# Optimization experiments

Measured on AMD Instinct MI355X. Metric: run time of the kernel, lower is better.

The kernel has to match this reference:

```python
import jax, jax.numpy as jnp
import numpy as np


def setup_inputs() -> dict:
    key = jax.random.key(0)
    k1, k2, k3, k4 = jax.random.split(key, 4)
    B1, N1, B2, N2, D = 64, 128, 64, 128, 128
    v1 = jax.random.normal(k1, (B1, N1, D), dtype=jnp.float32)
    v2 = jax.random.normal(k2, (B2, N2, D), dtype=jnp.float32)
    sz1 = jax.random.randint(k3, (B1,), 0, 128, dtype=jnp.int64)
    sz2 = jax.random.randint(k4, (B2,), 0, 128, dtype=jnp.int64)
    return {"v1": v1, "sz1": sz1, "v2": v2, "sz2": sz2}


def reference(v1, sz1, v2, sz2):
    # v1: (B1, N1, D) padded node features; v2: (B2, N2, D)
    # Pairwise Euclidean distances dist[b1,b2,i,j] = ||v1[b1,i] - v2[b2,j]||
    # via the gemm identity instead of the original's 5D broadcast.
    x2 = jnp.sum(v1 * v1, axis=-1)                     # (B1, N1)
    y2 = jnp.sum(v2 * v2, axis=-1)                     # (B2, N2)
    xy = jnp.einsum('aid,bjd->abij', v1, v2)           # (B1, B2, N1, N2)
    sq = x2[:, None, :, None] + y2[None, :, None, :] - 2.0 * xy
    dist = jnp.sqrt(jnp.maximum(sq, 0.0))              # (B1, B2, N1, N2)

    N1, N2 = v1.shape[1], v2.shape[1]
    mask1 = jnp.arange(N1)[None, :] >= sz1[:, None]    # (B1, N1) padded v1 nodes
    mask2 = jnp.arange(N2)[None, :] >= sz2[:, None]    # (B2, N2) padded v2 nodes
    mask = mask1[:, None, :, None] | mask2[None, :, None, :]  # (B1, B2, N1, N2)

    # Original fills masked entries with the global max of the (unmasked) distances.
    maximum = dist.max()
    dm = jnp.where(mask, maximum, dist)

    bm1 = dm.min(axis=2)                               # min over v1 nodes -> (B1, B2, N2)
    bm2 = dm.min(axis=3)                               # min over v2 nodes -> (B1, B2, N1)
    bm1 = jnp.where(jnp.all(mask, axis=2), 0.0, bm1)   # zero fully-masked columns
    bm2 = jnp.where(jnp.all(mask, axis=3), 0.0, bm2)   # zero fully-masked rows

    return bm1.sum(axis=2) + bm2.sum(axis=2)           # (B1, B2)
```

## Files before the change

kernel.cpp:

```cpp
#include <hip/hip_runtime.h>
#include <math.h>


typedef __attribute__((ext_vector_type(8))) short short8;
typedef __attribute__((ext_vector_type(4))) float f32x4;
typedef unsigned int u32;
typedef unsigned short ushort_t;

static __device__ __forceinline__ ushort_t f32_to_bf16_rne(float f) {
    u32 b = __float_as_uint(f);
    b += 0x7FFFu + ((b >> 16) & 1u);
    return (ushort_t)(b >> 16);
}

__global__ __launch_bounds__(256) void softhd_pre(
    const float* __restrict__ v1, const float* __restrict__ v2,
    ushort_t* __restrict__ v1b, ushort_t* __restrict__ v2b,
    float* __restrict__ x2g, float* __restrict__ y2g)
{
    int flat = blockIdx.x * 256 + threadIdx.x;
    int c = flat & 15;
    int r = (flat >> 4) & 127;
    int b = (flat >> 11) & 63;
    int t = flat >> 17;

    const float* src = (t ? v2 : v1) + ((size_t)((b << 7) + r) << 7) + c * 8;
    char* dstp = (char*)((t ? v2b : v1b) + ((size_t)b << 14));

    float4 q0 = *(const float4*)(src);
    float4 q1 = *(const float4*)(src + 4);

    ushort_t h[8];
    h[0] = f32_to_bf16_rne(q0.x); h[1] = f32_to_bf16_rne(q0.y);
    h[2] = f32_to_bf16_rne(q0.z); h[3] = f32_to_bf16_rne(q0.w);
    h[4] = f32_to_bf16_rne(q1.x); h[5] = f32_to_bf16_rne(q1.y);
    h[6] = f32_to_bf16_rne(q1.z); h[7] = f32_to_bf16_rne(q1.w);

    float p = 0.f;
#pragma unroll
    for (int k = 0; k < 8; ++k) {
        float fv = __uint_as_float((u32)h[k] << 16);
        p += fv * fv;
    }

    uint4 w;
    w.x = (u32)h[0] | ((u32)h[1] << 16);
    w.y = (u32)h[2] | ((u32)h[3] << 16);
    w.z = (u32)h[4] | ((u32)h[5] << 16);
    w.w = (u32)h[6] | ((u32)h[7] << 16);

    int off = ((c >> 2) << 13) + ((r >> 3) << 9) + ((c & 3) << 7) + ((r & 7) << 4);
    *(uint4*)(dstp + off) = w;

    p += __shfl_xor(p, 1);
    p += __shfl_xor(p, 2);
    p += __shfl_xor(p, 4);
    p += __shfl_xor(p, 8);
    if (c == 0) (t ? y2g : x2g)[(b << 7) + r] = p;
}

__global__ __launch_bounds__(256, 4) void softhd_mfma(
    const ushort_t* __restrict__ v1b, const ushort_t* __restrict__ v2b,
    const float* __restrict__ x2g, const float* __restrict__ y2g,
    const int* __restrict__ sz1, const int* __restrict__ sz2,
    float* __restrict__ out)
{
    __shared__ __align__(16) ushort_t sb[2][2][4096];
    __shared__ float sx2[128], sy2[128];
    __shared__ u32 sbm1[128], sbm2[128];
    __shared__ float swsum[4];

    const int tid = threadIdx.x;
    const int lane = tid & 63;
    const int wid = tid >> 6;
    const int bid = ((blockIdx.x & 7) << 9) | (blockIdx.x >> 3);
    const int b1 = bid >> 6, b2 = bid & 63;

    const char* gp0 = (const char*)(v1b + ((size_t)b1 << 14));
    const char* gp1 = (const char*)(v2b + ((size_t)b2 << 14));

#define STAGE(d, q)                                                          \
    {                                                                        \
        _Pragma("unroll")                                                    \
        for (int e = 0; e < 2; ++e) {                                        \
            int m16 = ((e << 8) + tid) << 4;                                 \
            __builtin_amdgcn_global_load_lds(                                \
                (const __attribute__((address_space(1))) u32*)(gp0 + ((q) << 13) + m16), \
                (__attribute__((address_space(3))) u32*)((char*)&sb[d][0][0] + m16),     \
                16, 0, 0);                                                   \
            __builtin_amdgcn_global_load_lds(                                \
                (const __attribute__((address_space(1))) u32*)(gp1 + ((q) << 13) + m16), \
                (__attribute__((address_space(3))) u32*)((char*)&sb[d][1][0] + m16),     \
                16, 0, 0);                                                   \
        }                                                                    \
    }

    STAGE(0, 0);

    const int n1 = min(max(sz1[b1], 0), 128);
    const int n2 = min(max(sz2[b2], 0), 128);

    if (tid < 128) {
        sx2[tid] = x2g[(b1 << 7) + tid];
        sbm1[tid] = 0x7F800000u;
    } else {
        sy2[tid - 128] = y2g[(b2 << 7) + (tid - 128)];
        sbm2[tid - 128] = 0x7F800000u;
    }
    __syncthreads();

    const int qr = wid >> 1, qc = wid & 1;
    const int ibase = qr << 6, jbase = qc << 6;
    const int rf = lane & 15, kg = lane >> 4;

    int aoff[4], boff[4];
#pragma unroll
    for (int f = 0; f < 4; ++f) {
        int ra = ibase + (f << 4) + rf;
        int rb = jbase + (f << 4) + rf;
        aoff[f] = ((ra >> 3) << 8) + (kg << 6) + ((ra & 7) << 3);
        boff[f] = ((rb >> 3) << 8) + (kg << 6) + ((rb & 7) << 3);
    }

    f32x4 acc[4][4];
#pragma unroll
    for (int fi = 0; fi < 4; ++fi)
#pragma unroll
        for (int fj = 0; fj < 4; ++fj)
            acc[fi][fj] = (f32x4){0.f, 0.f, 0.f, 0.f};

#pragma unroll
    for (int q = 0; q < 4; ++q) {
        const int d = q & 1;
        if (q < 3) STAGE(d ^ 1, q + 1);
        short8 a[4], b[4];
#pragma unroll
        for (int f = 0; f < 4; ++f) {
            a[f] = *(const short8*)(&sb[d][0][0] + aoff[f]);
            b[f] = *(const short8*)(&sb[d][1][0] + boff[f]);
        }
#pragma unroll
        for (int fi = 0; fi < 4; ++fi)
#pragma unroll
            for (int fj = 0; fj < 4; ++fj)
                acc[fi][fj] = __builtin_amdgcn_mfma_f32_16x16x32_bf16(
                    a[fi], b[fj], acc[fi][fj], 0, 0, 0);
        __syncthreads();
    }
#undef STAGE

    const float INF = __builtin_inff();

    float xie[16], yje[4];
#pragma unroll
    for (int t = 0; t < 16; ++t) {
        int i = ibase + ((t >> 2) << 4) + (kg << 2) + (t & 3);
        xie[t] = (i < n1) ? sx2[i] : INF;
    }
#pragma unroll
    for (int fj = 0; fj < 4; ++fj) {
        int j = jbase + (fj << 4) + rf;
        yje[fj] = (j < n2) ? sy2[j] : INF;
    }

    float minj[4], mini[16];
#pragma unroll
    for (int fj = 0; fj < 4; ++fj) minj[fj] = INF;
#pragma unroll
    for (int t = 0; t < 16; ++t) mini[t] = INF;

#pragma unroll
    for (int fi = 0; fi < 4; ++fi) {
        float u[4][4];
#pragma unroll
        for (int fj = 0; fj < 4; ++fj)
#pragma unroll
            for (int q = 0; q < 4; ++q)
                u[fj][q] = fmaf(acc[fi][fj][q], -2.f, xie[fi * 4 + q] + yje[fj]);
#pragma unroll
        for (int fj = 0; fj < 4; ++fj) {
            minj[fj] = fminf(fminf(minj[fj], u[fj][0]), u[fj][1]);
            minj[fj] = fminf(fminf(minj[fj], u[fj][2]), u[fj][3]);
        }
#pragma unroll
        for (int q = 0; q < 4; ++q) {
            float mt = mini[fi * 4 + q];
            mt = fminf(fminf(mt, u[0][q]), u[1][q]);
            mt = fminf(fminf(mt, u[2][q]), u[3][q]);
            mini[fi * 4 + q] = mt;
        }
    }

#pragma unroll
    for (int k = 0; k < 4; ++k) {
        const int d = 1 << k;
        const bool hi = (lane >> k) & 1;
#pragma unroll
        for (int base = 0; base < 16; base += 2 * (1 << k)) {
            float pa = fminf(mini[base], __shfl_xor(mini[base], d));
            float pb = fminf(mini[base + d], __shfl_xor(mini[base + d], d));
            mini[base] = hi ? pb : pa;
        }
    }
    {
        float dmin = __builtin_amdgcn_sqrtf(fmaxf(mini[0], 0.f));
        int i = ibase + ((rf >> 2) << 4) + (kg << 2) + (rf & 3);
        atomicMin(&sbm2[i], __float_as_uint(dmin));
    }

#pragma unroll
    for (int k = 0; k < 2; ++k) {
        const int d = 16 << k;
        const bool hi = (lane >> (4 + k)) & 1;
#pragma unroll
        for (int base = 0; base < 4; base += 2 * (1 << k)) {
            float pa = fminf(minj[base], __shfl_xor(minj[base], d));
            float pb = fminf(minj[base + (1 << k)],
                             __shfl_xor(minj[base + (1 << k)], d));
            minj[base] = hi ? pb : pa;
        }
    }
    {
        float dmin = __builtin_amdgcn_sqrtf(fmaxf(minj[0], 0.f));
        atomicMin(&sbm1[jbase + lane], __float_as_uint(dmin));
    }
    __syncthreads();

    float v = 0.f;
    if (tid < 128) {
        if (n1 > 0 && tid < n2) v += __uint_as_float(sbm1[tid]);
        if (n2 > 0 && tid < n1) v += __uint_as_float(sbm2[tid]);
    }
#pragma unroll
    for (int off = 32; off >= 1; off >>= 1) v += __shfl_down(v, off);
    if (lane == 0) swsum[wid] = v;
    __syncthreads();
    if (tid == 0) out[bid] = swsum[0] + swsum[1] + swsum[2] + swsum[3];
}

extern "C" void kernel_launch(void* const* d_in, const int* in_sizes, int n_in,
                              void* d_out, int out_size, void* d_ws, size_t ws_size,
                              hipStream_t stream) {
    const float* v1  = (const float*)d_in[0];
    const int*   sz1 = (const int*)d_in[1];
    const float* v2  = (const float*)d_in[2];
    const int*   sz2 = (const int*)d_in[3];
    float* out = (float*)d_out;
    (void)in_sizes; (void)n_in; (void)out_size; (void)ws_size;

    char* ws = (char*)d_ws;
    ushort_t* v1b = (ushort_t*)ws;
    ushort_t* v2b = (ushort_t*)(ws + (2u << 20));
    float*    x2g = (float*)(ws + (4u << 20));
    float*    y2g = x2g + 64 * 128;

    softhd_pre<<<dim3(1024), dim3(256), 0, stream>>>(v1, v2, v1b, v2b, x2g, y2g);
    softhd_mfma<<<dim3(4096), dim3(256), 0, stream>>>(v1b, v2b, x2g, y2g,
                                                      sz1, sz2, out);
}
```

Measured before the change: 36.55 us.

## Keep v1 tile in registers and loop each block over four v2 batches

Each block now handles one b1 against four b2 batches. The A operand (v1 tile) is loaded once straight from global memory into registers, and only the v2 tiles are streamed through double-buffered LDS in half-K chunks. The epilogue min-reduction runs inside the loop after each b2, which amortizes v1 loads and per-block setup over four outputs and cuts the grid from 4096 blocks to 1024. In exchange, register pressure rises (64 extra VGPRs for the A fragments), occupancy drops (launch bounds lowered to 3), and the epilogue is serialized with the MFMA work inside each block.

```diff
diff --git a/kernel.cpp b/kernel.cpp
--- a/kernel.cpp
+++ b/kernel.cpp
@@ -59,183 +59,192 @@
     if (c == 0) (t ? y2g : x2g)[(b << 7) + r] = p;
 }
 
-__global__ __launch_bounds__(256, 4) void softhd_mfma(
+__global__ __launch_bounds__(256, 3) void softhd_mfma(
     const ushort_t* __restrict__ v1b, const ushort_t* __restrict__ v2b,
     const float* __restrict__ x2g, const float* __restrict__ y2g,
     const int* __restrict__ sz1, const int* __restrict__ sz2,
     float* __restrict__ out)
 {
-    __shared__ __align__(16) ushort_t sb[2][2][4096];
-    __shared__ float sx2[128], sy2[128];
-    __shared__ u32 sbm1[128], sbm2[128];
-    __shared__ float swsum[4];
+    __shared__ __align__(16) ushort_t sB[2][8192];
+    __shared__ float sx2[128];
+    __shared__ float sy2[4][128];
+    __shared__ u32 sbm1[4][128];
+    __shared__ u32 sbm2[4][128];
 
     const int tid = threadIdx.x;
     const int lane = tid & 63;
     const int wid = tid >> 6;
-    const int bid = ((blockIdx.x & 7) << 9) | (blockIdx.x >> 3);
-    const int b1 = bid >> 6, b2 = bid & 63;
-
-    const char* gp0 = (const char*)(v1b + ((size_t)b1 << 14));
-    const char* gp1 = (const char*)(v2b + ((size_t)b2 << 14));
-
-#define STAGE(d, q)                                                          \
-    {                                                                        \
-        _Pragma("unroll")                                                    \
-        for (int e = 0; e < 2; ++e) {                                        \
-            int m16 = ((e << 8) + tid) << 4;                                 \
-            __builtin_amdgcn_global_load_lds(                                \
-                (const __attribute__((address_space(1))) u32*)(gp0 + ((q) << 13) + m16), \
-                (__attribute__((address_space(3))) u32*)((char*)&sb[d][0][0] + m16),     \
-                16, 0, 0);                                                   \
-            __builtin_amdgcn_global_load_lds(                                \
-                (const __attribute__((address_space(1))) u32*)(gp1 + ((q) << 13) + m16), \
-                (__attribute__((address_space(3))) u32*)((char*)&sb[d][1][0] + m16),     \
-                16, 0, 0);                                                   \
-        }                                                                    \
-    }
-
-    STAGE(0, 0);
-
-    const int n1 = min(max(sz1[b1], 0), 128);
-    const int n2 = min(max(sz2[b2], 0), 128);
-
-    if (tid < 128) {
-        sx2[tid] = x2g[(b1 << 7) + tid];
-        sbm1[tid] = 0x7F800000u;
-    } else {
-        sy2[tid - 128] = y2g[(b2 << 7) + (tid - 128)];
-        sbm2[tid - 128] = 0x7F800000u;
-    }
-    __syncthreads();
+    const int bid = ((blockIdx.x & 7) << 7) | (blockIdx.x >> 3);
+    const int b1 = bid >> 4;
+    const int b2base = (bid & 15) << 2;
+
+#define STAGE(dbuf, b2l, h)                                                   \
+    {                                                                         \
+        const char* _g = (const char*)(v2b + ((size_t)(b2base + (b2l)) << 14))\
+                         + ((h) << 14);                                       \
+        _Pragma("unroll")                                                     \
+        for (int e = 0; e < 4; ++e) {                                         \
+            int m16 = ((e << 8) + tid) << 4;                                  \
+            __builtin_amdgcn_global_load_lds(                                 \
+                (const __attribute__((address_space(1))) u32*)(_g + m16),     \
+                (__attribute__((address_space(3))) u32*)((char*)&sB[dbuf][0] + m16), \
+                16, 0, 0);                                                    \
+        }                                                                     \
+    }
+
+    STAGE(0, 0, 0);
 
     const int qr = wid >> 1, qc = wid & 1;
     const int ibase = qr << 6, jbase = qc << 6;
     const int rf = lane & 15, kg = lane >> 4;
 
-    int aoff[4], boff[4];
-#pragma unroll
-    for (int f = 0; f < 4; ++f) {
-        int ra = ibase + (f << 4) + rf;
-        int rb = jbase + (f << 4) + rf;
-        aoff[f] = ((ra >> 3) << 8) + (kg << 6) + ((ra & 7) << 3);
-        boff[f] = ((rb >> 3) << 8) + (kg << 6) + ((rb & 7) << 3);
-    }
+    short8 afr[4][4];
+    {
+        const char* gA = (const char*)(v1b + ((size_t)b1 << 14));
+        const int base0 = (((ibase + rf) >> 3) << 9) + (kg << 7) + ((rf & 7) << 4);
+#pragma unroll
+        for (int f = 0; f < 4; ++f)
+#pragma unroll
+            for (int q = 0; q < 4; ++q)
+                afr[f][q] = *(const short8*)(gA + base0 + (f << 10) + (q << 13));
+    }
+
+    if (tid < 128) sx2[tid] = x2g[(b1 << 7) + tid];
+#pragma unroll
+    for (int k = 0; k < 2; ++k) {
+        ((float*)sy2)[tid + (k << 8)] = y2g[(b2base << 7) + tid + (k << 8)];
+        ((u32*)sbm1)[tid + (k << 8)] = 0x7F800000u;
+        ((u32*)sbm2)[tid + (k << 8)] = 0x7F800000u;
+    }
+
+    const int n1 = min(max(sz1[b1], 0), 128);
+    int n2v[4];
+#pragma unroll
+    for (int z = 0; z < 4; ++z) n2v[z] = min(max(sz2[b2base + z], 0), 128);
+
+    __syncthreads();
+
+    const int boff0 = (((jbase + rf) >> 3) << 9) + (kg << 7) + ((rf & 7) << 4);
+    const float INF = __builtin_inff();
 
     f32x4 acc[4][4];
-#pragma unroll
-    for (int fi = 0; fi < 4; ++fi)
-#pragma unroll
-        for (int fj = 0; fj < 4; ++fj)
-            acc[fi][fj] = (f32x4){0.f, 0.f, 0.f, 0.f};
-
-#pragma unroll
-    for (int q = 0; q < 4; ++q) {
-        const int d = q & 1;
-        if (q < 3) STAGE(d ^ 1, q + 1);
-        short8 a[4], b[4];
-#pragma unroll
-        for (int f = 0; f < 4; ++f) {
-            a[f] = *(const short8*)(&sb[d][0][0] + aoff[f]);
-            b[f] = *(const short8*)(&sb[d][1][0] + boff[f]);
-        }
-#pragma unroll
-        for (int fi = 0; fi < 4; ++fi)
+
+#pragma unroll
+    for (int t = 0; t < 8; ++t) {
+        const int b2l = t >> 1, h = t & 1, d = t & 1;
+        if (t < 7) STAGE(d ^ 1, (t + 1) >> 1, (t + 1) & 1);
+        if (h == 0) {
+#pragma unroll
+            for (int fi = 0; fi < 4; ++fi)
+#pragma unroll
+                for (int fj = 0; fj < 4; ++fj)
+                    acc[fi][fj] = (f32x4){0.f, 0.f, 0.f, 0.f};
+        }
+#pragma unroll
+        for (int qq = 0; qq < 2; ++qq) {
+            const int q = h * 2 + qq;
+            short8 bfr[4];
 #pragma unroll
             for (int fj = 0; fj < 4; ++fj)
-                acc[fi][fj] = __builtin_amdgcn_mfma_f32_16x16x32_bf16(
-                    a[fi], b[fj], acc[fi][fj], 0, 0, 0);
+                bfr[fj] = *(const short8*)((const char*)&sB[d][0]
+                                           + (qq << 13) + (fj << 10) + boff0);
+#pragma unroll
+            for (int fi = 0; fi < 4; ++fi)
+#pragma unroll
+                for (int fj = 0; fj < 4; ++fj)
+                    acc[fi][fj] = __builtin_amdgcn_mfma_f32_16x16x32_bf16(
+                        afr[fi][q], bfr[fj], acc[fi][fj], 0, 0, 0);
+        }
+        if (h == 1) {
+            float yje[4];
+#pragma unroll
+            for (int fj = 0; fj < 4; ++fj) {
+                int j = jbase + (fj << 4) + rf;
+                yje[fj] = (j < n2v[b2l]) ? sy2[b2l][j] : INF;
+            }
+            float minj[4] = {INF, INF, INF, INF};
+            float mini[16];
+#pragma unroll
+            for (int z = 0; z < 16; ++z) mini[z] = INF;
+
+#pragma unroll
+            for (int fi = 0; fi < 4; ++fi) {
+                float4 xs = *(const float4*)&sx2[ibase + (fi << 4) + (kg << 2)];
+                float xie[4];
+#pragma unroll
+                for (int qe = 0; qe < 4; ++qe) {
+                    int i = ibase + (fi << 4) + (kg << 2) + qe;
+                    xie[qe] = (i < n1) ? ((const float*)&xs)[qe] : INF;
+                }
+#pragma unroll
+                for (int fj = 0; fj < 4; ++fj) {
+                    float u0 = fmaf(acc[fi][fj][0], -2.f, xie[0] + yje[fj]);
+                    float u1 = fmaf(acc[fi][fj][1], -2.f, xie[1] + yje[fj]);
+                    float u2 = fmaf(acc[fi][fj][2], -2.f, xie[2] + yje[fj]);
+                    float u3 = fmaf(acc[fi][fj][3], -2.f, xie[3] + yje[fj]);
+                    minj[fj] = fminf(fminf(fminf(minj[fj], u0), u1),
+                                     fminf(u2, u3));
+                    mini[(fi << 2) + 0] = fminf(mini[(fi << 2) + 0], u0);
+                    mini[(fi << 2) + 1] = fminf(mini[(fi << 2) + 1], u1);
+                    mini[(fi << 2) + 2] = fminf(mini[(fi << 2) + 2], u2);
+                    mini[(fi << 2) + 3] = fminf(mini[(fi << 2) + 3], u3);
+                }
+            }
+
+#pragma unroll
+            for (int k = 0; k < 4; ++k) {
+                const int dd = 1 << k;
+                const bool hi = (lane >> k) & 1;
+#pragma unroll
+                for (int base = 0; base < 16; base += 2 * (1 << k)) {
+                    float pa = fminf(mini[base], __shfl_xor(mini[base], dd));
+                    float pb = fminf(mini[base + dd],
+                                     __shfl_xor(mini[base + dd], dd));
+                    mini[base] = hi ? pb : pa;
+                }
+            }
+            {
+                float dmin = __builtin_amdgcn_sqrtf(fmaxf(mini[0], 0.f));
+                int i = ibase + ((rf >> 2) << 4) + (kg << 2) + (rf & 3);
+                atomicMin(&sbm2[b2l][i], __float_as_uint(dmin));
+            }
+#pragma unroll
+            for (int k = 0; k < 2; ++k) {
+                const int dd = 16 << k;
+                const bool hi = (lane >> (4 + k)) & 1;
+#pragma unroll
+                for (int base = 0; base < 4; base += 2 * (1 << k)) {
+                    float pa = fminf(minj[base], __shfl_xor(minj[base], dd));
+                    float pb = fminf(minj[base + (1 << k)],
+                                     __shfl_xor(minj[base + (1 << k)], dd));
+                    minj[base] = hi ? pb : pa;
+                }
+            }
+            {
+                float dmin = __builtin_amdgcn_sqrtf(fmaxf(minj[0], 0.f));
+                atomicMin(&sbm1[b2l][jbase + lane], __float_as_uint(dmin));
+            }
+        }
         __syncthreads();
     }
 #undef STAGE
 
-    const float INF = __builtin_inff();
-
-    float xie[16], yje[4];
-#pragma unroll
-    for (int t = 0; t < 16; ++t) {
-        int i = ibase + ((t >> 2) << 4) + (kg << 2) + (t & 3);
-        xie[t] = (i < n1) ? sx2[i] : INF;
-    }
-#pragma unroll
-    for (int fj = 0; fj < 4; ++fj) {
-        int j = jbase + (fj << 4) + rf;
-        yje[fj] = (j < n2) ? sy2[j] : INF;
-    }
-
-    float minj[4], mini[16];
-#pragma unroll
-    for (int fj = 0; fj < 4; ++fj) minj[fj] = INF;
-#pragma unroll
-    for (int t = 0; t < 16; ++t) mini[t] = INF;
-
-#pragma unroll
-    for (int fi = 0; fi < 4; ++fi) {
-        float u[4][4];
-#pragma unroll
-        for (int fj = 0; fj < 4; ++fj)
-#pragma unroll
-            for (int q = 0; q < 4; ++q)
-                u[fj][q] = fmaf(acc[fi][fj][q], -2.f, xie[fi * 4 + q] + yje[fj]);
-#pragma unroll
-        for (int fj = 0; fj < 4; ++fj) {
-            minj[fj] = fminf(fminf(minj[fj], u[fj][0]), u[fj][1]);
-            minj[fj] = fminf(fminf(minj[fj], u[fj][2]), u[fj][3]);
-        }
-#pragma unroll
-        for (int q = 0; q < 4; ++q) {
-            float mt = mini[fi * 4 + q];
-            mt = fminf(fminf(mt, u[0][q]), u[1][q]);
-            mt = fminf(fminf(mt, u[2][q]), u[3][q]);
-            mini[fi * 4 + q] = mt;
-        }
-    }
-
-#pragma unroll
-    for (int k = 0; k < 4; ++k) {
-        const int d = 1 << k;
-        const bool hi = (lane >> k) & 1;
-#pragma unroll
-        for (int base = 0; base < 16; base += 2 * (1 << k)) {
-            float pa = fminf(mini[base], __shfl_xor(mini[base], d));
-            float pb = fminf(mini[base + d], __shfl_xor(mini[base + d], d));
-            mini[base] = hi ? pb : pa;
-        }
-    }
     {
-        float dmin = __builtin_amdgcn_sqrtf(fmaxf(mini[0], 0.f));
-        int i = ibase + ((rf >> 2) << 4) + (kg << 2) + (rf & 3);
-        atomicMin(&sbm2[i], __float_as_uint(dmin));
-    }
-
-#pragma unroll
-    for (int k = 0; k < 2; ++k) {
-        const int d = 16 << k;
-        const bool hi = (lane >> (4 + k)) & 1;
-#pragma unroll
-        for (int base = 0; base < 4; base += 2 * (1 << k)) {
-            float pa = fminf(minj[base], __shfl_xor(minj[base], d));
-            float pb = fminf(minj[base + (1 << k)],
-                             __shfl_xor(minj[base + (1 << k)], d));
-            minj[base] = hi ? pb : pa;
-        }
-    }
-    {
-        float dmin = __builtin_amdgcn_sqrtf(fmaxf(minj[0], 0.f));
-        atomicMin(&sbm1[jbase + lane], __float_as_uint(dmin));
-    }
-    __syncthreads();
-
-    float v = 0.f;
-    if (tid < 128) {
-        if (n1 > 0 && tid < n2) v += __uint_as_float(sbm1[tid]);
-        if (n2 > 0 && tid < n1) v += __uint_as_float(sbm2[tid]);
-    }
-#pragma unroll
-    for (int off = 32; off >= 1; off >>= 1) v += __shfl_down(v, off);
-    if (lane == 0) swsum[wid] = v;
-    __syncthreads();
-    if (tid == 0) out[bid] = swsum[0] + swsum[1] + swsum[2] + swsum[3];
+        const int nn2 = n2v[wid];
+        float v = 0.f;
+        const int e0 = lane, e1 = lane + 64;
+        if (n1 > 0) {
+            if (e0 < nn2) v += __uint_as_float(sbm1[wid][e0]);
+            if (e1 < nn2) v += __uint_as_float(sbm1[wid][e1]);
+        }
+        if (nn2 > 0) {
+            if (e0 < n1) v += __uint_as_float(sbm2[wid][e0]);
+            if (e1 < n1) v += __uint_as_float(sbm2[wid][e1]);
+        }
+#pragma unroll
+        for (int off = 32; off >= 1; off >>= 1) v += __shfl_down(v, off);
+        if (lane == 0) out[(b1 << 6) + b2base + wid] = v;
+    }
 }
 
 extern "C" void kernel_launch(void* const* d_in, const int* in_sizes, int n_in,
@@ -255,6 +264,6 @@
     float*    y2g = x2g + 64 * 128;
 
     softhd_pre<<<dim3(1024), dim3(256), 0, stream>>>(v1, v2, v1b, v2b, x2g, y2g);
-    softhd_mfma<<<dim3(4096), dim3(256), 0, stream>>>(v1b, v2b, x2g, y2g,
+    softhd_mfma<<<dim3(1024), dim3(256), 0, stream>>>(v1b, v2b, x2g, y2g,
                                                       sz1, sz2, out);
 }
```

New measurement: 52.80 us. 44.4% more time.

## Prefetch two LDS stages ahead with explicit vmcnt waits and raw barriers

Applied to the files above, without the earlier changes.

Replaces the double-buffered K loop with a hand-scheduled pipeline. Two stages are issued up front and partial `s_waitcnt vmcnt(4)` waits are used, so the next stage's global-to-LDS loads stay in flight while the current stage is computed. The scalar/shared init loads move ahead of the first stage, and raw s_barrier replaces __syncthreads to avoid the full vmcnt(0) drain. The risk is correctness: it depends on the exact count of outstanding vector memory ops, including the x2/y2/sz loads issued before the stages, and on the plain-LDS writes of sx2/sbm being visible without a full waitcnt.

```diff
diff --git a/kernel.cpp b/kernel.cpp
--- a/kernel.cpp
+++ b/kernel.cpp
@@ -78,6 +78,18 @@
 
     const char* gp0 = (const char*)(v1b + ((size_t)b1 << 14));
     const char* gp1 = (const char*)(v2b + ((size_t)b2 << 14));
+
+    const int n1 = min(max(sz1[b1], 0), 128);
+    const int n2 = min(max(sz2[b2], 0), 128);
+
+    if (tid < 128) {
+        sx2[tid] = x2g[(b1 << 7) + tid];
+        sbm1[tid] = 0x7F800000u;
+    } else {
+        sy2[tid - 128] = y2g[(b2 << 7) + (tid - 128)];
+        sbm2[tid - 128] = 0x7F800000u;
+    }
+    asm volatile("" ::: "memory");
 
 #define STAGE(d, q)                                                          \
     {                                                                        \
@@ -94,20 +106,12 @@
                 16, 0, 0);                                                   \
         }                                                                    \
     }
+#define WAITV4()  asm volatile("s_waitcnt vmcnt(4)" ::: "memory")
+#define WAITV0()  asm volatile("s_waitcnt vmcnt(0)" ::: "memory")
+#define BAR()     asm volatile("s_barrier" ::: "memory")
 
     STAGE(0, 0);
-
-    const int n1 = min(max(sz1[b1], 0), 128);
-    const int n2 = min(max(sz2[b2], 0), 128);
-
-    if (tid < 128) {
-        sx2[tid] = x2g[(b1 << 7) + tid];
-        sbm1[tid] = 0x7F800000u;
-    } else {
-        sy2[tid - 128] = y2g[(b2 << 7) + (tid - 128)];
-        sbm2[tid - 128] = 0x7F800000u;
-    }
-    __syncthreads();
+    STAGE(1, 1);
 
     const int qr = wid >> 1, qc = wid & 1;
     const int ibase = qr << 6, jbase = qc << 6;
@@ -129,25 +133,39 @@
         for (int fj = 0; fj < 4; ++fj)
             acc[fi][fj] = (f32x4){0.f, 0.f, 0.f, 0.f};
 
-#pragma unroll
-    for (int q = 0; q < 4; ++q) {
-        const int d = q & 1;
-        if (q < 3) STAGE(d ^ 1, q + 1);
-        short8 a[4], b[4];
-#pragma unroll
-        for (int f = 0; f < 4; ++f) {
-            a[f] = *(const short8*)(&sb[d][0][0] + aoff[f]);
-            b[f] = *(const short8*)(&sb[d][1][0] + boff[f]);
-        }
-#pragma unroll
-        for (int fi = 0; fi < 4; ++fi)
-#pragma unroll
-            for (int fj = 0; fj < 4; ++fj)
-                acc[fi][fj] = __builtin_amdgcn_mfma_f32_16x16x32_bf16(
-                    a[fi], b[fj], acc[fi][fj], 0, 0, 0);
-        __syncthreads();
-    }
+#define COMPUTE(d)                                                           \
+    {                                                                        \
+        short8 a[4], b[4];                                                   \
+        _Pragma("unroll")                                                    \
+        for (int f = 0; f < 4; ++f) {                                        \
+            a[f] = *(const short8*)(&sb[d][0][0] + aoff[f]);                 \
+            b[f] = *(const short8*)(&sb[d][1][0] + boff[f]);                 \
+        }                                                                    \
+        _Pragma("unroll")                                                    \
+        for (int fi = 0; fi < 4; ++fi)                                       \
+            _Pragma("unroll")                                                \
+            for (int fj = 0; fj < 4; ++fj)                                   \
+                acc[fi][fj] = __builtin_amdgcn_mfma_f32_16x16x32_bf16(       \
+                    a[fi], b[fj], acc[fi][fj], 0, 0, 0);                     \
+    }
+
+    WAITV4(); BAR();
+    COMPUTE(0);
+    BAR(); STAGE(0, 2);
+    WAITV4(); BAR();
+    COMPUTE(1);
+    BAR(); STAGE(1, 3);
+    WAITV4(); BAR();
+    COMPUTE(0);
+    BAR();
+    WAITV0(); BAR();
+    COMPUTE(1);
+
+#undef COMPUTE
 #undef STAGE
+#undef WAITV4
+#undef WAITV0
+#undef BAR
 
     const float INF = __builtin_inff();
 
```

Measured after the change: 36.02 us. About the same (-1.5%).
